# Kernel tuning notes

Hardware: AMD Instinct MI355X
Metric: run time of the kernel (lower is better)

## Reference

```python
import jax, jax.numpy as jnp
import numpy as np


def setup_inputs() -> dict:
    key = jax.random.key(0)
    k1, k2 = jax.random.split(key)
    B, G, P = 64, 4999, 50
    raw_gene_expr = jax.random.normal(k1, (B, G), dtype=jnp.float32)
    # binary pathway membership matrix, mimics torch.randint(0, 2, (P, G)).float()
    pathway_gene_matrix = (jax.random.uniform(k2, (P, G)) < 0.5).astype(jnp.float32)
    return {"raw_gene_expr": raw_gene_expr, "pathway_gene_matrix": pathway_gene_matrix}


def reference(raw_gene_expr, pathway_gene_matrix):
    """Vectorized ssGSEA enrichment (compute_pathway_activations0).

    raw_gene_expr:        [B, G] float
    pathway_gene_matrix:  [P, G] binary float
    returns:              [B, P] signed max-deviation enrichment scores
    """
    B, G = raw_gene_expr.shape
    P = pathway_gene_matrix.shape[0]

    # Sort genes per sample in descending expression order
    order = jnp.argsort(-raw_gene_expr, axis=1)                      # [B, G]
    sorted_expr = jnp.take_along_axis(raw_gene_expr, order, axis=1)  # [B, G]

    # hit[b, p, i] = 1 if gene at sorted position i belongs to pathway p
    hit = (pathway_gene_matrix[:, order] > 0)                        # [P, B, G]
    hit = jnp.transpose(hit, (1, 0, 2)).astype(raw_gene_expr.dtype)  # [B, P, G]

    size = jnp.sum(pathway_gene_matrix > 0, axis=1).astype(raw_gene_expr.dtype)  # [P]

    # Weighted hit increments: |expr|^0.25 over hits, normalized per (sample, pathway)
    w = (jnp.abs(sorted_expr) ** 0.25)[:, None, :] * hit             # [B, P, G]
    s = jnp.sum(w, axis=-1, keepdims=True)
    w = jnp.where(s > 0, w / jnp.where(s > 0, s, 1.0), w)

    cum_hit = jnp.cumsum(w, axis=-1)                                 # [B, P, G]
    denom = jnp.maximum(G - size, 1.0)[None, :, None]                # guard size==G
    cum_miss = jnp.cumsum((1.0 - hit) / denom, axis=-1)              # [B, P, G]

    running = cum_hit - cum_miss                                     # [B, P, G]
    pos = jnp.argmax(jnp.abs(running), axis=-1)                      # [B, P]
    # signed max deviation == running value at the argmax of |running|
    es = jnp.take_along_axis(running, pos[..., None], axis=-1)[..., 0]  # [B, P]
    es = jnp.where(size[None, :] > 0, es, 0.0)
    return es
```

## Files before the change

kernel.cpp:

```cpp
#include <hip/hip_runtime.h>
#include <math.h>

typedef unsigned long long ull;

constexpr int Bc = 64;
constexpr int Gc = 4999;
constexpr int Pc = 50;

constexpr int RUN   = 1024;
constexpr int NRUN  = 5;
constexpr int NPAD  = NRUN * RUN;
constexpr int LPW3  = 41;
constexpr int HALF0 = 64 * LPW3;
constexpr ull PADKEY = 0xFFFFFFFFFFFFFFFFull;

__device__ __forceinline__ ull shfl_xor64(ull v, int lm) {
    int lo = __shfl_xor((int)(unsigned)(v & 0xFFFFFFFFull), lm, 64);
    int hi = __shfl_xor((int)(unsigned)(v >> 32), lm, 64);
    return ((ull)(unsigned)hi << 32) | (unsigned)lo;
}

__global__ __launch_bounds__(256) void chunk_sort(
    const float* __restrict__ expr, const float* __restrict__ pathway,
    ull* __restrict__ runs, ull* __restrict__ pbits, int P, int G)
{
    __shared__ ull key[RUN];
    const int r = blockIdx.x, b = blockIdx.y, tid = threadIdx.x;
    const int base = tid * 4;
    const float* row = expr + (size_t)b * G;

    ull v[4];
#pragma unroll
    for (int o = 0; o < 4; ++o) {
        int i = r * RUN + base + o;
        if (i < G) {
            unsigned u = __float_as_uint(row[i]);
            unsigned m = (u >> 31) ? ~u : (u | 0x80000000u);
            v[o] = ((ull)(~m) << 32) | (unsigned)i;
        } else {
            v[o] = PADKEY;
        }
    }

    for (int kk = 2; kk <= RUN; kk <<= 1) {
        const int j0 = kk >> 1;
        if (j0 >= 256) {
#pragma unroll
            for (int o = 0; o < 4; ++o) key[base + o] = v[o];
            __syncthreads();
            for (int j = j0; j >= 256; j >>= 1) {
#pragma unroll
                for (int t = tid; t < RUN / 2; t += 256) {
                    int i  = ((t & ~(j - 1)) << 1) | (t & (j - 1));
                    int ix = i | j;
                    ull a = key[i], c = key[ix];
                    bool up = ((i & kk) == 0);
                    if ((a > c) == up) { key[i] = c; key[ix] = a; }
                }
                __syncthreads();
            }
#pragma unroll
            for (int o = 0; o < 4; ++o) v[o] = key[base + o];
        }
        int jstart = (j0 > 128) ? 128 : j0;
        for (int j = jstart; j >= 4; j >>= 1) {
            int lm = j >> 2;
            bool takeMin = (((tid & lm) == 0) == ((base & kk) == 0));
#pragma unroll
            for (int o = 0; o < 4; ++o) {
                ull c = shfl_xor64(v[o], lm);
                ull mn = (v[o] < c) ? v[o] : c;
                ull mx = (v[o] < c) ? c : v[o];
                v[o] = takeMin ? mn : mx;
            }
        }
#pragma unroll
        for (int j = 2; j >= 1; j >>= 1) {
            if (j < kk) {
#pragma unroll
                for (int o = 0; o < 4; ++o) {
                    if ((o & j) == 0) {
                        bool up = (((base + o) & kk) == 0);
                        ull a = v[o], c = v[o | j];
                        if ((a > c) == up) { v[o] = c; v[o | j] = a; }
                    }
                }
            }
        }
    }

    ull* dst = runs + ((size_t)b * NRUN + r) * RUN;
#pragma unroll
    for (int o = 0; o < 4; ++o) dst[base + o] = v[o];

    if (r == 0) {
        int g = b * 256 + tid;
        if (g < G) {
            ull m = 0;
#pragma unroll
            for (int p = 0; p < Pc; ++p)
                if (pathway[(size_t)p * G + g] > 0.0f) m |= (1ull << p);
            pbits[g] = m;
        }
    }
}

__global__ __launch_bounds__(1024) void rank_scatter(
    const ull* __restrict__ runs, const ull* __restrict__ pbits,
    float* __restrict__ wqout, ull* __restrict__ pbout, int G)
{
    __shared__ ull runsLDS[NPAD];
    const int rg = blockIdx.x, b = blockIdx.y, tid = threadIdx.x;

    const ull* rowruns = runs + (size_t)b * NPAD;
    for (int i = tid; i < NPAD; i += 1024) runsLDS[i] = rowruns[i];
    __syncthreads();

    const int e = rg * 1024 + tid;
    const ull keyv = runsLDS[e];
    if (keyv == PADKEY) return;

    const int idx = (int)(unsigned)(keyv & 0xFFFFFFFFu);
    const ull pb = pbits[idx];

    const int run = e >> 10;
    int rank = e & 1023;
#pragma unroll
    for (int rr = 0; rr < NRUN; ++rr) {
        if (rr == run) continue;
        const ull* arr = &runsLDS[rr * RUN];
        int pos = 0;
#pragma unroll
        for (int s = RUN; s >= 1; s >>= 1) {
            int np = pos + s;
            if (np <= RUN && arr[np - 1] < keyv) pos = np;
        }
        rank += pos;
    }

    unsigned m = ~((unsigned)(keyv >> 32));
    unsigned absbits = ((m >> 31) ? m : ~m) & 0x7FFFFFFFu;
    float av = __uint_as_float(absbits);
    wqout[(size_t)b * G + rank] = sqrtf(sqrtf(av));
    pbout[(size_t)b * G + rank] = pb;
}

__global__ __launch_bounds__(512) void es_kernel(
    const float* __restrict__ wq, const ull* __restrict__ pb64,
    float* __restrict__ out, int B, int P, int G)
{
    __shared__ float    swq[Gc];
    __shared__ unsigned sm32[Gc];
    __shared__ double   cSW[4][2][4];
    __shared__ int      cSH[4][2][4];
    __shared__ double   cBV[4][2][4];
    __shared__ double   cBR[4][2][4];
    __shared__ int      cBI[4][2][4];

    const int pg = blockIdx.x;
    const int b  = blockIdx.y;
    const int tid = threadIdx.x;
    const int pbeg = pg * 13;
    const int pend = (pbeg + 13 < P) ? (pbeg + 13) : P;

    for (int i = tid; i < G; i += 512) {
        swq[i]  = wq[(size_t)b * G + i];
        sm32[i] = (unsigned)(pb64[(size_t)b * G + i] >> pbeg);
    }
    __syncthreads();

    const int lane = tid & 63;
    const int w  = tid >> 6;
    const int qg = w >> 1;
    const int h  = w & 1;
    const int sh4 = qg * 4;

    const int lg = h * 64 + lane;
    const int start = lg * LPW3;
    int cnt = G - start;
    cnt = (cnt < 0) ? 0 : ((cnt > LPW3) ? LPW3 : cnt);

    double sw[4] = {0.0, 0.0, 0.0, 0.0};
    int sh[4] = {0, 0, 0, 0};
    for (int k = 0; k < cnt; ++k) {
        int s = start + k;
        unsigned nib = (sm32[s] >> sh4) & 15u;
        double wv = (double)swq[s];
#pragma unroll
        for (int q = 0; q < 4; ++q) {
            if ((nib >> q) & 1u) { sw[q] += wv; sh[q]++; }
        }
    }
#pragma unroll
    for (int q = 0; q < 4; ++q) {
        double s_ = sw[q]; int c_ = sh[q];
#pragma unroll
        for (int off = 1; off < 64; off <<= 1) {
            s_ += __shfl_xor(s_, off, 64);
            c_ += __shfl_xor(c_, off, 64);
        }
        if (lane == 0) { cSW[qg][h][q] = s_; cSH[qg][h][q] = c_; }
    }
    __syncthreads();

    double norm[4], inv_denom[4], running[4];
    int shtot[4];
#pragma unroll
    for (int q = 0; q < 4; ++q) {
        double s0 = cSW[qg][0][q], s1 = cSW[qg][1][q];
        int    c0 = cSH[qg][0][q], c1 = cSH[qg][1][q];
        double st = s0 + s1;
        int    ct = c0 + c1;
        shtot[q]     = ct;
        norm[q]      = (st > 0.0) ? 1.0 / st : 1.0;
        inv_denom[q] = 1.0 / fmax((double)(G - ct), 1.0);
        double off1 = s0 * norm[q] - (double)(HALF0 - c0) * inv_denom[q];
        double csum = sw[q] * norm[q] - (double)(cnt - sh[q]) * inv_denom[q];
        double x = csum;
#pragma unroll
        for (int off = 1; off < 64; off <<= 1) {
            double vv = __shfl_up(x, off, 64);
            if (lane >= off) x += vv;
        }
        running[q] = x - csum + (h ? off1 : 0.0);
    }

    double bestv[4] = {-1.0, -1.0, -1.0, -1.0};
    double bestr[4] = {0.0, 0.0, 0.0, 0.0};
    int besti[4] = {0x7FFFFFFF, 0x7FFFFFFF, 0x7FFFFFFF, 0x7FFFFFFF};
    for (int k = 0; k < cnt; ++k) {
        int s = start + k;
        unsigned nib = (sm32[s] >> sh4) & 15u;
        double wv = (double)swq[s];
#pragma unroll
        for (int q = 0; q < 4; ++q) {
            running[q] += ((nib >> q) & 1u) ? wv * norm[q] : -inv_denom[q];
            double a = fabs(running[q]);
            if (a > bestv[q]) { bestv[q] = a; bestr[q] = running[q]; besti[q] = s; }
        }
    }
#pragma unroll
    for (int q = 0; q < 4; ++q) {
#pragma unroll
        for (int off = 1; off < 64; off <<= 1) {
            double ov  = __shfl_xor(bestv[q], off, 64);
            double orr = __shfl_xor(bestr[q], off, 64);
            int    oi  = __shfl_xor(besti[q], off, 64);
            if (ov > bestv[q] || (ov == bestv[q] && oi < besti[q])) {
                bestv[q] = ov; bestr[q] = orr; besti[q] = oi;
            }
        }
        if (lane == 0) { cBV[qg][h][q] = bestv[q]; cBR[qg][h][q] = bestr[q]; cBI[qg][h][q] = besti[q]; }
    }
    __syncthreads();

    if (h == 0 && lane == 0) {
#pragma unroll
        for (int q = 0; q < 4; ++q) {
            double v0 = cBV[qg][0][q], v1 = cBV[qg][1][q];
            double r_ = (v1 > v0) ? cBR[qg][1][q] : cBR[qg][0][q];
            int p = pbeg + sh4 + q;
            if (p < pend)
                out[(size_t)b * P + p] = (shtot[q] > 0) ? (float)r_ : 0.0f;
        }
    }
}

extern "C" void kernel_launch(void* const* d_in, const int* in_sizes, int n_in,
                              void* d_out, int out_size, void* d_ws, size_t ws_size,
                              hipStream_t stream) {
    const float* expr    = (const float*)d_in[0];
    const float* pathway = (const float*)d_in[1];
    float* out = (float*)d_out;

    char* ws = (char*)d_ws;
    ull*   pbits = (ull*)ws;
    ull*   runs  = (ull*)(ws + 40960);
    float* wqa   = (float*)(ws + 2662400);
    ull*   pb64  = (ull*)(ws + 3942144);

    chunk_sort<<<dim3(NRUN, Bc), dim3(256), 0, stream>>>(
        expr, pathway, runs, pbits, Pc, Gc);
    rank_scatter<<<dim3(NRUN, Bc), dim3(1024), 0, stream>>>(runs, pbits, wqa, pb64, Gc);
    es_kernel<<<dim3(4, Bc), dim3(512), 0, stream>>>(
        wqa, pb64, out, Bc, Pc, Gc);
}
```

Baseline: 103.7 us.

## Double thread counts in chunk sort and ES scan to shorten serial chains

The chunk sort now uses 512 threads holding 2 keys each instead of 256 threads with 4. This moves more bitonic stages into cross-lane shuffles and one in-register swap. The ES kernel now splits the gene range into four segments per pathway group instead of two, using 1024 threads with 21 genes per lane. Cross-segment prefix offsets are combined through shared memory. The aim is to halve the per-thread sequential scan length, at the cost of more shared-memory barrier work and larger blocks that may lower occupancy.

```diff
diff --git a/kernel.cpp b/kernel.cpp
--- a/kernel.cpp
+++ b/kernel.cpp
@@ -10,8 +10,8 @@
 constexpr int RUN   = 1024;
 constexpr int NRUN  = 5;
 constexpr int NPAD  = NRUN * RUN;
-constexpr int LPW3  = 41;
-constexpr int HALF0 = 64 * LPW3;
+constexpr int LPW4  = 21;
+constexpr int QSPAN = 64 * LPW4;
 constexpr ull PADKEY = 0xFFFFFFFFFFFFFFFFull;
 
 __device__ __forceinline__ ull shfl_xor64(ull v, int lm) {
@@ -20,18 +20,18 @@
     return ((ull)(unsigned)hi << 32) | (unsigned)lo;
 }
 
-__global__ __launch_bounds__(256) void chunk_sort(
+__global__ __launch_bounds__(512) void chunk_sort(
     const float* __restrict__ expr, const float* __restrict__ pathway,
     ull* __restrict__ runs, ull* __restrict__ pbits, int P, int G)
 {
     __shared__ ull key[RUN];
     const int r = blockIdx.x, b = blockIdx.y, tid = threadIdx.x;
-    const int base = tid * 4;
+    const int base = tid * 2;
     const float* row = expr + (size_t)b * G;
 
-    ull v[4];
-#pragma unroll
-    for (int o = 0; o < 4; ++o) {
+    ull v[2];
+#pragma unroll
+    for (int o = 0; o < 2; ++o) {
         int i = r * RUN + base + o;
         if (i < G) {
             unsigned u = __float_as_uint(row[i]);
@@ -44,13 +44,12 @@
 
     for (int kk = 2; kk <= RUN; kk <<= 1) {
         const int j0 = kk >> 1;
-        if (j0 >= 256) {
-#pragma unroll
-            for (int o = 0; o < 4; ++o) key[base + o] = v[o];
+        if (j0 >= 128) {
+#pragma unroll
+            for (int o = 0; o < 2; ++o) key[base + o] = v[o];
             __syncthreads();
-            for (int j = j0; j >= 256; j >>= 1) {
-#pragma unroll
-                for (int t = tid; t < RUN / 2; t += 256) {
+            for (int j = j0; j >= 128; j >>= 1) {
+                for (int t = tid; t < RUN / 2; t += 512) {
                     int i  = ((t & ~(j - 1)) << 1) | (t & (j - 1));
                     int ix = i | j;
                     ull a = key[i], c = key[ix];
@@ -60,41 +59,32 @@
                 __syncthreads();
             }
 #pragma unroll
-            for (int o = 0; o < 4; ++o) v[o] = key[base + o];
-        }
-        int jstart = (j0 > 128) ? 128 : j0;
-        for (int j = jstart; j >= 4; j >>= 1) {
-            int lm = j >> 2;
+            for (int o = 0; o < 2; ++o) v[o] = key[base + o];
+        }
+        int jstart = (j0 > 64) ? 64 : j0;
+        for (int j = jstart; j >= 2; j >>= 1) {
+            int lm = j >> 1;
             bool takeMin = (((tid & lm) == 0) == ((base & kk) == 0));
 #pragma unroll
-            for (int o = 0; o < 4; ++o) {
+            for (int o = 0; o < 2; ++o) {
                 ull c = shfl_xor64(v[o], lm);
                 ull mn = (v[o] < c) ? v[o] : c;
                 ull mx = (v[o] < c) ? c : v[o];
                 v[o] = takeMin ? mn : mx;
             }
         }
-#pragma unroll
-        for (int j = 2; j >= 1; j >>= 1) {
-            if (j < kk) {
-#pragma unroll
-                for (int o = 0; o < 4; ++o) {
-                    if ((o & j) == 0) {
-                        bool up = (((base + o) & kk) == 0);
-                        ull a = v[o], c = v[o | j];
-                        if ((a > c) == up) { v[o] = c; v[o | j] = a; }
-                    }
-                }
-            }
+        {
+            bool up = ((base & kk) == 0);
+            if ((v[0] > v[1]) == up) { ull t = v[0]; v[0] = v[1]; v[1] = t; }
         }
     }
 
     ull* dst = runs + ((size_t)b * NRUN + r) * RUN;
 #pragma unroll
-    for (int o = 0; o < 4; ++o) dst[base + o] = v[o];
+    for (int o = 0; o < 2; ++o) dst[base + o] = v[o];
 
     if (r == 0) {
-        int g = b * 256 + tid;
+        int g = b * 512 + tid;
         if (g < G) {
             ull m = 0;
 #pragma unroll
@@ -145,17 +135,16 @@
     pbout[(size_t)b * G + rank] = pb;
 }
 
-__global__ __launch_bounds__(512) void es_kernel(
+__global__ __launch_bounds__(1024) void es_kernel(
     const float* __restrict__ wq, const ull* __restrict__ pb64,
     float* __restrict__ out, int B, int P, int G)
 {
     __shared__ float    swq[Gc];
     __shared__ unsigned sm32[Gc];
-    __shared__ double   cSW[4][2][4];
-    __shared__ int      cSH[4][2][4];
-    __shared__ double   cBV[4][2][4];
-    __shared__ double   cBR[4][2][4];
-    __shared__ int      cBI[4][2][4];
+    __shared__ double   cSW[4][4][4];
+    __shared__ int      cSH[4][4][4];
+    __shared__ double   cBV[4][4][4];
+    __shared__ double   cBR[4][4][4];
 
     const int pg = blockIdx.x;
     const int b  = blockIdx.y;
@@ -163,7 +152,7 @@
     const int pbeg = pg * 13;
     const int pend = (pbeg + 13 < P) ? (pbeg + 13) : P;
 
-    for (int i = tid; i < G; i += 512) {
+    for (int i = tid; i < G; i += 1024) {
         swq[i]  = wq[(size_t)b * G + i];
         sm32[i] = (unsigned)(pb64[(size_t)b * G + i] >> pbeg);
     }
@@ -171,14 +160,14 @@
 
     const int lane = tid & 63;
     const int w  = tid >> 6;
-    const int qg = w >> 1;
-    const int h  = w & 1;
+    const int qg = w >> 2;
+    const int h  = w & 3;
     const int sh4 = qg * 4;
 
     const int lg = h * 64 + lane;
-    const int start = lg * LPW3;
+    const int start = lg * LPW4;
     int cnt = G - start;
-    cnt = (cnt < 0) ? 0 : ((cnt > LPW3) ? LPW3 : cnt);
+    cnt = (cnt < 0) ? 0 : ((cnt > LPW4) ? LPW4 : cnt);
 
     double sw[4] = {0.0, 0.0, 0.0, 0.0};
     int sh[4] = {0, 0, 0, 0};
@@ -203,18 +192,27 @@
     }
     __syncthreads();
 
+    int Qc[4];
+#pragma unroll
+    for (int hh = 0; hh < 4; ++hh) {
+        int c = G - hh * QSPAN;
+        Qc[hh] = (c < 0) ? 0 : ((c > QSPAN) ? QSPAN : c);
+    }
+
     double norm[4], inv_denom[4], running[4];
     int shtot[4];
 #pragma unroll
     for (int q = 0; q < 4; ++q) {
-        double s0 = cSW[qg][0][q], s1 = cSW[qg][1][q];
-        int    c0 = cSH[qg][0][q], c1 = cSH[qg][1][q];
-        double st = s0 + s1;
-        int    ct = c0 + c1;
+        double st = 0.0; int ct = 0;
+#pragma unroll
+        for (int hh = 0; hh < 4; ++hh) { st += cSW[qg][hh][q]; ct += cSH[qg][hh][q]; }
         shtot[q]     = ct;
         norm[q]      = (st > 0.0) ? 1.0 / st : 1.0;
         inv_denom[q] = 1.0 / fmax((double)(G - ct), 1.0);
-        double off1 = s0 * norm[q] - (double)(HALF0 - c0) * inv_denom[q];
+        double offq = 0.0;
+        for (int hh = 0; hh < h; ++hh)
+            offq += cSW[qg][hh][q] * norm[q]
+                  - (double)(Qc[hh] - cSH[qg][hh][q]) * inv_denom[q];
         double csum = sw[q] * norm[q] - (double)(cnt - sh[q]) * inv_denom[q];
         double x = csum;
 #pragma unroll
@@ -222,7 +220,7 @@
             double vv = __shfl_up(x, off, 64);
             if (lane >= off) x += vv;
         }
-        running[q] = x - csum + (h ? off1 : 0.0);
+        running[q] = x - csum + offq;
     }
 
     double bestv[4] = {-1.0, -1.0, -1.0, -1.0};
@@ -250,18 +248,23 @@
                 bestv[q] = ov; bestr[q] = orr; besti[q] = oi;
             }
         }
-        if (lane == 0) { cBV[qg][h][q] = bestv[q]; cBR[qg][h][q] = bestr[q]; cBI[qg][h][q] = besti[q]; }
+        if (lane == 0) { cBV[qg][h][q] = bestv[q]; cBR[qg][h][q] = bestr[q]; }
     }
     __syncthreads();
 
     if (h == 0 && lane == 0) {
 #pragma unroll
         for (int q = 0; q < 4; ++q) {
-            double v0 = cBV[qg][0][q], v1 = cBV[qg][1][q];
-            double r_ = (v1 > v0) ? cBR[qg][1][q] : cBR[qg][0][q];
+            double bv = cBV[qg][0][q];
+            double br = cBR[qg][0][q];
+#pragma unroll
+            for (int hh = 1; hh < 4; ++hh) {
+                double v_ = cBV[qg][hh][q];
+                if (v_ > bv) { bv = v_; br = cBR[qg][hh][q]; }
+            }
             int p = pbeg + sh4 + q;
             if (p < pend)
-                out[(size_t)b * P + p] = (shtot[q] > 0) ? (float)r_ : 0.0f;
+                out[(size_t)b * P + p] = (shtot[q] > 0) ? (float)br : 0.0f;
         }
     }
 }
@@ -279,9 +282,9 @@
     float* wqa   = (float*)(ws + 2662400);
     ull*   pb64  = (ull*)(ws + 3942144);
 
-    chunk_sort<<<dim3(NRUN, Bc), dim3(256), 0, stream>>>(
+    chunk_sort<<<dim3(NRUN, Bc), dim3(512), 0, stream>>>(
         expr, pathway, runs, pbits, Pc, Gc);
     rank_scatter<<<dim3(NRUN, Bc), dim3(1024), 0, stream>>>(runs, pbits, wqa, pb64, Gc);
-    es_kernel<<<dim3(4, Bc), dim3(512), 0, stream>>>(
+    es_kernel<<<dim3(4, Bc), dim3(1024), 0, stream>>>(
         wqa, pb64, out, Bc, Pc, Gc);
 }
```

Result: no change. 105.5 us (+1.7%).

## Sort each 1024-key run in one wavefront and interleave weight with pathway bits

Applied to the files above, without the earlier changes.

The block-level bitonic sort is replaced by a per-wavefront sort. Each lane holds 16 keys in registers and exchanges them with shuffles, so the LDS stages and block barriers are gone. Loads are vectorised as float4 and the pathway bitmask build is spread across the new grid. The per-gene weight and pathway bitmask are packed into one 16-byte record, so the ES kernel does one wide load per gene instead of two separate streams. The trade-off is four times fewer threads in the sort, more register pressure and longer per-lane serial compare chains.

```diff
diff --git a/kernel.cpp b/kernel.cpp
--- a/kernel.cpp
+++ b/kernel.cpp
@@ -10,8 +10,10 @@
 constexpr int RUN   = 1024;
 constexpr int NRUN  = 5;
 constexpr int NPAD  = NRUN * RUN;
-constexpr int LPW3  = 41;
-constexpr int HALF0 = 64 * LPW3;
+constexpr int NCHUNK = NRUN * Bc;
+constexpr int EW   = 16;
+constexpr int LPW  = 41;
+constexpr int HALF0 = 64 * LPW;
 constexpr ull PADKEY = 0xFFFFFFFFFFFFFFFFull;
 
 __device__ __forceinline__ ull shfl_xor64(ull v, int lm) {
@@ -20,65 +22,79 @@
     return ((ull)(unsigned)hi << 32) | (unsigned)lo;
 }
 
-__global__ __launch_bounds__(256) void chunk_sort(
+__global__ __launch_bounds__(256) void wave_sort(
     const float* __restrict__ expr, const float* __restrict__ pathway,
     ull* __restrict__ runs, ull* __restrict__ pbits, int P, int G)
 {
-    __shared__ ull key[RUN];
-    const int r = blockIdx.x, b = blockIdx.y, tid = threadIdx.x;
-    const int base = tid * 4;
+    const int tid  = threadIdx.x;
+    const int lane = tid & 63;
+    const int w    = tid >> 6;
+
+    {
+        int g = blockIdx.x * 256 + tid;
+        if (g < G) {
+            ull m = 0;
+#pragma unroll
+            for (int p = 0; p < Pc; ++p)
+                if (pathway[(size_t)p * G + g] > 0.0f) m |= (1ull << p);
+            pbits[g] = m;
+        }
+    }
+
+    const int C = blockIdx.x * 4 + w;
+    const int b = C / NRUN, r = C % NRUN;
+    const int base = lane * EW;
     const float* row = expr + (size_t)b * G;
-
-    ull v[4];
-#pragma unroll
-    for (int o = 0; o < 4; ++o) {
-        int i = r * RUN + base + o;
-        if (i < G) {
-            unsigned u = __float_as_uint(row[i]);
-            unsigned m = (u >> 31) ? ~u : (u | 0x80000000u);
-            v[o] = ((ull)(~m) << 32) | (unsigned)i;
-        } else {
-            v[o] = PADKEY;
-        }
-    }
-
+    const int gbase = r * RUN + base;
+
+    ull v[EW];
+    if (gbase + EW <= G) {
+        const float4* row4 = (const float4*)(row + r * RUN);
+#pragma unroll
+        for (int f = 0; f < 4; ++f) {
+            float4 x = row4[lane * 4 + f];
+            float xs[4] = {x.x, x.y, x.z, x.w};
+#pragma unroll
+            for (int c = 0; c < 4; ++c) {
+                int o = f * 4 + c;
+                unsigned u = __float_as_uint(xs[c]);
+                unsigned m = (u >> 31) ? ~u : (u | 0x80000000u);
+                v[o] = ((ull)(~m) << 32) | (unsigned)(gbase + o);
+            }
+        }
+    } else {
+#pragma unroll
+        for (int o = 0; o < EW; ++o) {
+            int i = gbase + o;
+            if (i < G) {
+                unsigned u = __float_as_uint(row[i]);
+                unsigned m = (u >> 31) ? ~u : (u | 0x80000000u);
+                v[o] = ((ull)(~m) << 32) | (unsigned)i;
+            } else {
+                v[o] = PADKEY;
+            }
+        }
+    }
+
+#pragma unroll 1
     for (int kk = 2; kk <= RUN; kk <<= 1) {
         const int j0 = kk >> 1;
-        if (j0 >= 256) {
-#pragma unroll
-            for (int o = 0; o < 4; ++o) key[base + o] = v[o];
-            __syncthreads();
-            for (int j = j0; j >= 256; j >>= 1) {
-#pragma unroll
-                for (int t = tid; t < RUN / 2; t += 256) {
-                    int i  = ((t & ~(j - 1)) << 1) | (t & (j - 1));
-                    int ix = i | j;
-                    ull a = key[i], c = key[ix];
-                    bool up = ((i & kk) == 0);
-                    if ((a > c) == up) { key[i] = c; key[ix] = a; }
-                }
-                __syncthreads();
-            }
-#pragma unroll
-            for (int o = 0; o < 4; ++o) v[o] = key[base + o];
-        }
-        int jstart = (j0 > 128) ? 128 : j0;
-        for (int j = jstart; j >= 4; j >>= 1) {
-            int lm = j >> 2;
-            bool takeMin = (((tid & lm) == 0) == ((base & kk) == 0));
-#pragma unroll
-            for (int o = 0; o < 4; ++o) {
+        int jstart = (j0 > 512) ? 512 : j0;
+        for (int j = jstart; j >= EW; j >>= 1) {
+            int lm = j >> 4;
+            bool takeMin = (((lane & lm) == 0) == ((base & kk) == 0));
+#pragma unroll
+            for (int o = 0; o < EW; ++o) {
                 ull c = shfl_xor64(v[o], lm);
                 ull mn = (v[o] < c) ? v[o] : c;
                 ull mx = (v[o] < c) ? c : v[o];
                 v[o] = takeMin ? mn : mx;
             }
         }
-#pragma unroll
-        for (int j = 2; j >= 1; j >>= 1) {
+        for (int j = 8; j >= 1; j >>= 1) {
             if (j < kk) {
 #pragma unroll
-                for (int o = 0; o < 4; ++o) {
+                for (int o = 0; o < EW; ++o) {
                     if ((o & j) == 0) {
                         bool up = (((base + o) & kk) == 0);
                         ull a = v[o], c = v[o | j];
@@ -89,25 +105,17 @@
         }
     }
 
-    ull* dst = runs + ((size_t)b * NRUN + r) * RUN;
-#pragma unroll
-    for (int o = 0; o < 4; ++o) dst[base + o] = v[o];
-
-    if (r == 0) {
-        int g = b * 256 + tid;
-        if (g < G) {
-            ull m = 0;
-#pragma unroll
-            for (int p = 0; p < Pc; ++p)
-                if (pathway[(size_t)p * G + g] > 0.0f) m |= (1ull << p);
-            pbits[g] = m;
-        }
+    ulonglong2* dst2 = (ulonglong2*)(runs + (size_t)C * RUN);
+#pragma unroll
+    for (int o = 0; o < EW; o += 2) {
+        ulonglong2 t; t.x = v[o]; t.y = v[o + 1];
+        dst2[lane * (EW / 2) + o / 2] = t;
     }
 }
 
 __global__ __launch_bounds__(1024) void rank_scatter(
     const ull* __restrict__ runs, const ull* __restrict__ pbits,
-    float* __restrict__ wqout, ull* __restrict__ pbout, int G)
+    ulonglong2* __restrict__ wp, int G)
 {
     __shared__ ull runsLDS[NPAD];
     const int rg = blockIdx.x, b = blockIdx.y, tid = threadIdx.x;
@@ -141,13 +149,15 @@
     unsigned m = ~((unsigned)(keyv >> 32));
     unsigned absbits = ((m >> 31) ? m : ~m) & 0x7FFFFFFFu;
     float av = __uint_as_float(absbits);
-    wqout[(size_t)b * G + rank] = sqrtf(sqrtf(av));
-    pbout[(size_t)b * G + rank] = pb;
+    ulonglong2 t;
+    t.x = pb;
+    t.y = (ull)__float_as_uint(sqrtf(sqrtf(av)));
+    wp[(size_t)b * G + rank] = t;
 }
 
 __global__ __launch_bounds__(512) void es_kernel(
-    const float* __restrict__ wq, const ull* __restrict__ pb64,
-    float* __restrict__ out, int B, int P, int G)
+    const ulonglong2* __restrict__ wp, float* __restrict__ out,
+    int B, int P, int G)
 {
     __shared__ float    swq[Gc];
     __shared__ unsigned sm32[Gc];
@@ -155,7 +165,6 @@
     __shared__ int      cSH[4][2][4];
     __shared__ double   cBV[4][2][4];
     __shared__ double   cBR[4][2][4];
-    __shared__ int      cBI[4][2][4];
 
     const int pg = blockIdx.x;
     const int b  = blockIdx.y;
@@ -164,8 +173,9 @@
     const int pend = (pbeg + 13 < P) ? (pbeg + 13) : P;
 
     for (int i = tid; i < G; i += 512) {
-        swq[i]  = wq[(size_t)b * G + i];
-        sm32[i] = (unsigned)(pb64[(size_t)b * G + i] >> pbeg);
+        ulonglong2 t = wp[(size_t)b * G + i];
+        swq[i]  = __uint_as_float((unsigned)t.y);
+        sm32[i] = (unsigned)(t.x >> pbeg);
     }
     __syncthreads();
 
@@ -176,9 +186,9 @@
     const int sh4 = qg * 4;
 
     const int lg = h * 64 + lane;
-    const int start = lg * LPW3;
+    const int start = lg * LPW;
     int cnt = G - start;
-    cnt = (cnt < 0) ? 0 : ((cnt > LPW3) ? LPW3 : cnt);
+    cnt = (cnt < 0) ? 0 : ((cnt > LPW) ? LPW : cnt);
 
     double sw[4] = {0.0, 0.0, 0.0, 0.0};
     int sh[4] = {0, 0, 0, 0};
@@ -250,7 +260,7 @@
                 bestv[q] = ov; bestr[q] = orr; besti[q] = oi;
             }
         }
-        if (lane == 0) { cBV[qg][h][q] = bestv[q]; cBR[qg][h][q] = bestr[q]; cBI[qg][h][q] = besti[q]; }
+        if (lane == 0) { cBV[qg][h][q] = bestv[q]; cBR[qg][h][q] = bestr[q]; }
     }
     __syncthreads();
 
@@ -274,14 +284,13 @@
     float* out = (float*)d_out;
 
     char* ws = (char*)d_ws;
-    ull*   pbits = (ull*)ws;
-    ull*   runs  = (ull*)(ws + 40960);
-    float* wqa   = (float*)(ws + 2662400);
-    ull*   pb64  = (ull*)(ws + 3942144);
-
-    chunk_sort<<<dim3(NRUN, Bc), dim3(256), 0, stream>>>(
+    ull*        pbits = (ull*)ws;
+    ull*        runs  = (ull*)(ws + 40960);
+    ulonglong2* wp    = (ulonglong2*)(ws + 2662400);
+
+    wave_sort<<<dim3(NCHUNK / 4), dim3(256), 0, stream>>>(
         expr, pathway, runs, pbits, Pc, Gc);
-    rank_scatter<<<dim3(NRUN, Bc), dim3(1024), 0, stream>>>(runs, pbits, wqa, pb64, Gc);
+    rank_scatter<<<dim3(NRUN, Bc), dim3(1024), 0, stream>>>(runs, pbits, wp, Gc);
     es_kernel<<<dim3(4, Bc), dim3(512), 0, stream>>>(
-        wqa, pb64, out, Bc, Pc, Gc);
-}
+        wp, out, Bc, Pc, Gc);
+}
```

New measurement: 116.3 us. 12.1% more time.
